# Optimization experiments

Measured on AMD Instinct MI355X. Metric: run time of the kernel, lower is better.

The kernel has to match this reference:

```python
import jax, jax.numpy as jnp
import numpy as np

B, L, V = 4, 1024, 1280
N_EMBD, N_BIN, N_HID = 768, 8, 32
HORIZON = 10.0


def setup_inputs() -> dict:
    key = jax.random.key(0)
    k_h, k_age, k_gap, k_tgt, k_w1, k_w2 = jax.random.split(key, 6)
    h = jax.random.normal(k_h, (B, L, N_EMBD), dtype=jnp.float32)
    # ages increase along a trajectory; gaps in [0, 2) years
    age = jnp.sort(jax.random.uniform(k_age, (B, L), dtype=jnp.float32) * 80.0, axis=-1)
    targets_age = age + jax.random.uniform(k_gap, (B, L), dtype=jnp.float32) * 2.0
    delta_t = targets_age - age  # passed to forward but unused (as in torch source)
    targets = jax.random.randint(k_tgt, (B, L), 0, V, dtype=jnp.int32)
    W1 = jax.random.normal(k_w1, (N_EMBD, N_BIN * N_HID), dtype=jnp.float32) * 0.02
    W2 = jax.random.normal(k_w2, (N_HID, V), dtype=jnp.float32) * 0.02
    return {"h": h, "age": age, "targets_age": targets_age, "delta_t": delta_t,
            "targets": targets, "W1": W1, "W2": W2}


def _time_to_event(age, targets_age, targets):
    # delta_full[b,i,j] = targets_age[b,j] - age[b,i]
    delta_full = targets_age[:, None, :] - age[:, :, None]  # (B,L,L)
    i_idx = jnp.arange(L)
    # torch.triu(diagonal=0): keep targets[b,j] where j>=i, else 0
    upper = (i_idx[None, :] >= i_idx[:, None])  # (L,L) mask, col>=row
    targets_exp = jnp.where(upper[None, :, :], targets[:, None, :], 0)  # (B,L,L)
    # scatter-reduce amin of position index j into vocab slot targets_exp[b,i,j]
    # sentinel L plays the role of torch's -1 (min over srcs ignores it; src<=L-1)
    b_ix = jnp.arange(B)[:, None, None]
    r_ix = i_idx[None, :, None]
    src = jnp.broadcast_to(i_idx[None, None, :], (B, L, L)).astype(jnp.int32)
    token_index = jnp.full((B, L, V), L, dtype=jnp.int32)
    token_index = token_index.at[b_ix, r_ix, targets_exp].min(src)
    no_event = token_index == L
    token_index = jnp.where(no_event, L - 1, token_index)  # (B,L,V)
    tte = jnp.take_along_axis(delta_full, token_index, axis=-1)  # (B,L,V)
    return tte, no_event, token_index


def reference(h, age, targets_age, delta_t, targets, W1, W2):
    # two dense projections: (B,L,E) -> (B,L,n_bin,n_hid) -> (B,L,n_bin,V)
    x = jnp.einsum('ble,eo->blo', h, W1).reshape(B, L, N_BIN, N_HID)
    logits = jnp.einsum('blnh,hv->blnv', x, W2)
    tte, no_event, _ = _time_to_event(age, targets_age, targets)
    edges = jnp.linspace(0.0, HORIZON, N_BIN + 1)
    lo = edges[:-1][None, None, :, None]
    hi = edges[1:][None, None, :, None]
    t = tte[:, :, None, :]  # (B,L,1,V)
    censor_mask = ((t >= lo) & (t < hi)) | no_event[:, :, None, :]  # (B,L,n_bin,V)
    return logits, tte, censor_mask
```

## Files before the change

kernel.cpp:

```cpp
#include <hip/hip_runtime.h>
#include <hip/hip_bf16.h>

#define B_   4
#define L_   1024
#define V_   1280
#define NE_  768
#define NB_  8
#define NH_  32
#define NO_  (NB_*NH_)
#define BL_  (B_*L_)
#define M2_  (BL_*NB_)
#define NCH_ 64

typedef __attribute__((ext_vector_type(8))) short bf16x8;
typedef __attribute__((ext_vector_type(4))) float floatx4;

__device__ __forceinline__ unsigned short f2bf(float f) {
    unsigned int u = __float_as_uint(f);
    u += 0x7FFFu + ((u >> 16) & 1u);
    return (unsigned short)(u >> 16);
}

#define H4_N   (BL_*NE_/4)
#define W1T_N  (NO_*NE_)
#define W2T_N  (V_*NH_)
#define K0_TOT (H4_N + W1T_N + W2T_N)

__global__ __launch_bounds__(256) void k0_pack(const float* __restrict__ h,
                                               const float* __restrict__ W1,
                                               const float* __restrict__ W2,
                                               unsigned short* __restrict__ hb,
                                               unsigned short* __restrict__ W1T,
                                               unsigned short* __restrict__ W2T) {
    int id = blockIdx.x * 256 + threadIdx.x;
    if (id < H4_N) {
        float4 v = ((const float4*)h)[id];
        ushort4 o;
        o.x = f2bf(v.x); o.y = f2bf(v.y); o.z = f2bf(v.z); o.w = f2bf(v.w);
        ((ushort4*)hb)[id] = o;
    } else if (id < H4_N + W1T_N) {
        int j = id - H4_N;
        int o = j / NE_;
        int k = j - o * NE_;
        W1T[j] = f2bf(W1[(size_t)k * NO_ + o]);
    } else if (id < K0_TOT) {
        int j = id - H4_N - W1T_N;
        int v = j >> 5;
        int k = j & 31;
        W2T[j] = f2bf(W2[(size_t)k * V_ + v]);
    }
}

__global__ __launch_bounds__(256) void k1_gemm(const unsigned short* __restrict__ hb,
                                               const unsigned short* __restrict__ W1T,
                                               unsigned short* __restrict__ Xb) {
    __shared__ short A_lds[64][40];
    __shared__ short Bt_lds[64][40];

    const int t      = threadIdx.x;
    const int m0     = blockIdx.x * 64;
    const int n0     = blockIdx.y * 64;
    const int l      = t & 63;
    const int w      = t >> 6;
    const int lane15 = l & 15;
    const int quad   = l >> 4;

    const int srow = t >> 2;
    const int sq   = (t & 3) * 8;

    const unsigned short* aptr = hb  + (size_t)(m0 + srow) * NE_ + sq;
    const unsigned short* bptr = W1T + (size_t)(n0 + srow) * NE_ + sq;

    floatx4 acc[4];
#pragma unroll
    for (int i = 0; i < 4; ++i) acc[i] = (floatx4){0.f, 0.f, 0.f, 0.f};

    bf16x8 av = *(const bf16x8*)aptr;
    bf16x8 bv = *(const bf16x8*)bptr;

    for (int k0 = 0; k0 < NE_; k0 += 32) {
        __syncthreads();
        *(bf16x8*)&A_lds[srow][sq]  = av;
        *(bf16x8*)&Bt_lds[srow][sq] = bv;
        __syncthreads();
        if (k0 + 32 < NE_) {
            av = *(const bf16x8*)(aptr + k0 + 32);
            bv = *(const bf16x8*)(bptr + k0 + 32);
        }
        bf16x8 af = *(bf16x8*)&A_lds[w * 16 + lane15][quad * 8];
#pragma unroll
        for (int nt = 0; nt < 4; ++nt) {
            bf16x8 bf = *(bf16x8*)&Bt_lds[nt * 16 + lane15][quad * 8];
            acc[nt] = __builtin_amdgcn_mfma_f32_16x16x32_bf16(af, bf, acc[nt], 0, 0, 0);
        }
    }

    const int rbase = m0 + w * 16 + quad * 4;
#pragma unroll
    for (int nt = 0; nt < 4; ++nt)
#pragma unroll
        for (int r = 0; r < 4; ++r)
            Xb[(size_t)(rbase + r) * NO_ + n0 + nt * 16 + lane15] = f2bf(acc[nt][r]);
}

__global__ __launch_bounds__(256) void k2_logits(const unsigned short* __restrict__ Xb,
                                                 const unsigned short* __restrict__ W2T,
                                                 float* __restrict__ outL) {
    const int t      = threadIdx.x;
    const int m0     = blockIdx.x * 64;
    const int nt0    = blockIdx.y * 16;
    const int l      = t & 63;
    const int w      = t >> 6;
    const int lane15 = l & 15;
    const int quad   = l >> 4;

    const int m = m0 + w * 16 + lane15;
    const bf16x8 af = *(const bf16x8*)(Xb + (size_t)m * NH_ + quad * 8);

    const int rbase = m0 + w * 16 + quad * 4;

#pragma unroll 4
    for (int nt = nt0; nt < nt0 + 16; ++nt) {
        bf16x8 bf = *(const bf16x8*)(W2T + (size_t)(nt * 16 + lane15) * NH_ + quad * 8);
        floatx4 c = (floatx4){0.f, 0.f, 0.f, 0.f};
        c = __builtin_amdgcn_mfma_f32_16x16x32_bf16(af, bf, c, 0, 0, 0);
#pragma unroll
        for (int r = 0; r < 4; ++r)
            outL[(size_t)(rbase + r) * V_ + nt * 16 + lane15] = c[r];
    }
}

__global__ __launch_bounds__(256) void k3a_nxt(const int* __restrict__ targets,
                                               int* __restrict__ nxt) {
    const int b = blockIdx.x;
    const int v = blockIdx.y * 256 + threadIdx.x;
    __shared__ int tg[L_];
    for (int j = threadIdx.x; j < L_; j += 256) tg[j] = targets[(size_t)b * L_ + j];
    __syncthreads();
    int cur = L_;
    for (int j = L_ - 1; j >= 0; --j) {
        if ((j & 15) == 15)
            nxt[((size_t)b * NCH_ + (j >> 4)) * V_ + v] = cur;
        if (tg[j] == v) cur = j;
    }
}

__global__ __launch_bounds__(64) void k3b_out(const float* __restrict__ age,
                                              const float* __restrict__ tage,
                                              const int*   __restrict__ targets,
                                              const int*   __restrict__ nxt,
                                              float* __restrict__ outT,
                                              float* __restrict__ outM) {
    __shared__ float ta[L_];
    __shared__ int   tgc[16];
    __shared__ float agc[16];

    const int t  = threadIdx.x;
    const int vt = blockIdx.x;
    const int c  = blockIdx.y;
    const int b  = blockIdx.z;
    const int v0 = vt * 256 + t * 4;

    for (int j = t; j < L_; j += 64) ta[j] = tage[(size_t)b * L_ + j];
    if (t < 16) {
        tgc[t] = targets[(size_t)b * L_ + c * 16 + t];
        agc[t] = age[(size_t)b * L_ + c * 16 + t];
    }
    __syncthreads();

    int4 cur = *(const int4*)&nxt[((size_t)b * NCH_ + c) * V_ + v0];

    for (int ii = 15; ii >= 0; --ii) {
        const int   i  = c * 16 + ii;
        const int   ti = tgc[ii];
        const float ai = agc[ii];

        if (ti == v0 + 0) cur.x = i;
        if (ti == v0 + 1) cur.y = i;
        if (ti == v0 + 2) cur.z = i;
        if (ti == v0 + 3) cur.w = i;

        int ix = cur.x, iy = cur.y, iz = cur.z, iw = cur.w;
        if (v0 == 0 && i >= 1) ix = 0;
        const bool nex = (ix == L_), ney = (iy == L_), nez = (iz == L_), new_ = (iw == L_);

        float4 tt;
        tt.x = ta[nex ? L_ - 1 : ix] - ai;
        tt.y = ta[ney ? L_ - 1 : iy] - ai;
        tt.z = ta[nez ? L_ - 1 : iz] - ai;
        tt.w = ta[new_ ? L_ - 1 : iw] - ai;

        const size_t row = (size_t)(b * L_ + i);
        *(float4*)&outT[row * V_ + v0] = tt;

        const size_t mb = row * NB_ * V_ + v0;
#pragma unroll
        for (int n = 0; n < NB_; ++n) {
            const float lo = n * 1.25f;
            const float hi = (n + 1) * 1.25f;
            float4 m;
            m.x = ((tt.x >= lo && tt.x < hi) || nex)  ? 1.0f : 0.0f;
            m.y = ((tt.y >= lo && tt.y < hi) || ney)  ? 1.0f : 0.0f;
            m.z = ((tt.z >= lo && tt.z < hi) || nez)  ? 1.0f : 0.0f;
            m.w = ((tt.w >= lo && tt.w < hi) || new_) ? 1.0f : 0.0f;
            *(float4*)&outM[mb + (size_t)n * V_] = m;
        }
    }
}

extern "C" void kernel_launch(void* const* d_in, const int* in_sizes, int n_in,
                              void* d_out, int out_size, void* d_ws, size_t ws_size,
                              hipStream_t stream) {
    const float* h       = (const float*)d_in[0];
    const float* age     = (const float*)d_in[1];
    const float* tage    = (const float*)d_in[2];
    const int*   targets = (const int*)  d_in[4];
    const float* W1      = (const float*)d_in[5];
    const float* W2      = (const float*)d_in[6];

    float* out  = (float*)d_out;
    float* outL = out;
    float* outT = out + (size_t)BL_ * NB_ * V_;
    float* outM = outT + (size_t)BL_ * V_;

    char* ws = (char*)d_ws;
    unsigned short* hb  = (unsigned short*)(ws);
    unsigned short* W1T = (unsigned short*)(ws + 6291456);
    unsigned short* W2T = (unsigned short*)(ws + 6291456 + 393216);
    unsigned short* Xb  = (unsigned short*)(ws + 6291456 + 393216 + 81920);
    int*            nxt = (int*)(ws + 6291456 + 393216 + 81920 + 2097152);

    k0_pack  <<<(K0_TOT + 255) / 256, 256, 0, stream>>>(h, W1, W2, hb, W1T, W2T);
    k3a_nxt  <<<dim3(B_, V_/256), 256, 0, stream>>>(targets, nxt);
    k1_gemm  <<<dim3(BL_/64, NO_/64), 256, 0, stream>>>(hb, W1T, Xb);
    k2_logits<<<dim3(M2_/64, 5), 256, 0, stream>>>(Xb, W2T, outL);
    k3b_out  <<<dim3(5, NCH_, B_), 64, 0, stream>>>(age, tage, targets, nxt, outT, outM);
}
```

Measured before the change: 426.9 us.

## Merge independent kernels into fewer launches with block-index dispatch

Folds the next-occurrence scan into the pack kernel and the time-to-event/mask writer into the logits kernel. Each merged kernel dispatches on block index, so five launches become three. The tte/mask part now uses 256-thread blocks that each cover four chunks. This is meant to cut launch gaps and let the write-heavy mask output overlap with the logits stores, but it puts the serial scan blocks alongside the pack blocks and mixes work of different shapes in one grid.

```diff
diff --git a/kernel.cpp b/kernel.cpp
--- a/kernel.cpp
+++ b/kernel.cpp
@@ -25,14 +25,34 @@
 #define W1T_N  (NO_*NE_)
 #define W2T_N  (V_*NH_)
 #define K0_TOT (H4_N + W1T_N + W2T_N)
-
-__global__ __launch_bounds__(256) void k0_pack(const float* __restrict__ h,
+#define K0_BLK (K0_TOT/256)
+#define KA_BLK (K0_BLK + 20)
+
+__global__ __launch_bounds__(256) void kA_prep(const float* __restrict__ h,
                                                const float* __restrict__ W1,
                                                const float* __restrict__ W2,
+                                               const int*   __restrict__ targets,
                                                unsigned short* __restrict__ hb,
                                                unsigned short* __restrict__ W1T,
-                                               unsigned short* __restrict__ W2T) {
-    int id = blockIdx.x * 256 + threadIdx.x;
+                                               unsigned short* __restrict__ W2T,
+                                               int* __restrict__ nxt) {
+    const int bx = blockIdx.x;
+    const int t  = threadIdx.x;
+    if (bx < 20) {
+        __shared__ int tg[L_];
+        const int b = bx / 5;
+        const int v = (bx % 5) * 256 + t;
+        for (int j = t; j < L_; j += 256) tg[j] = targets[(size_t)b * L_ + j];
+        __syncthreads();
+        int cur = L_;
+        for (int j = L_ - 1; j >= 0; --j) {
+            if ((j & 15) == 15)
+                nxt[((size_t)b * NCH_ + (j >> 4)) * V_ + v] = cur;
+            if (tg[j] == v) cur = j;
+        }
+        return;
+    }
+    int id = (bx - 20) * 256 + t;
     if (id < H4_N) {
         float4 v = ((const float4*)h)[id];
         ushort4 o;
@@ -103,12 +123,85 @@
             Xb[(size_t)(rbase + r) * NO_ + n0 + nt * 16 + lane15] = f2bf(acc[nt][r]);
 }
 
-__global__ __launch_bounds__(256) void k2_logits(const unsigned short* __restrict__ Xb,
-                                                 const unsigned short* __restrict__ W2T,
-                                                 float* __restrict__ outL) {
-    const int t      = threadIdx.x;
-    const int m0     = blockIdx.x * 64;
-    const int nt0    = blockIdx.y * 16;
+#define KC_TTE 320
+#define KC_BLK (KC_TTE + 512*5)
+
+__global__ __launch_bounds__(256) void kC_out(const float* __restrict__ age,
+                                              const float* __restrict__ tage,
+                                              const int*   __restrict__ targets,
+                                              const int*   __restrict__ nxt,
+                                              const unsigned short* __restrict__ Xb,
+                                              const unsigned short* __restrict__ W2T,
+                                              float* __restrict__ outL,
+                                              float* __restrict__ outT,
+                                              float* __restrict__ outM) {
+    const int bx = blockIdx.x;
+    const int t  = threadIdx.x;
+
+    if (bx < KC_TTE) {
+        __shared__ float ta[L_];
+        __shared__ int   tgc[64];
+        __shared__ float agc[64];
+
+        const int vt   = bx % 5;
+        const int c0   = (bx / 5) & 15;
+        const int b    = bx / 80;
+        const int w    = t >> 6;
+        const int lane = t & 63;
+        const int c    = c0 * 4 + w;
+        const int v0   = vt * 256 + lane * 4;
+
+        for (int j = t; j < L_; j += 256) ta[j] = tage[(size_t)b * L_ + j];
+        if (t < 64) {
+            tgc[t] = targets[(size_t)b * L_ + c0 * 64 + t];
+            agc[t] = age[(size_t)b * L_ + c0 * 64 + t];
+        }
+        __syncthreads();
+
+        int4 cur = *(const int4*)&nxt[((size_t)b * NCH_ + c) * V_ + v0];
+
+        for (int ii = 15; ii >= 0; --ii) {
+            const int   i  = c * 16 + ii;
+            const int   ti = tgc[w * 16 + ii];
+            const float ai = agc[w * 16 + ii];
+
+            if (ti == v0 + 0) cur.x = i;
+            if (ti == v0 + 1) cur.y = i;
+            if (ti == v0 + 2) cur.z = i;
+            if (ti == v0 + 3) cur.w = i;
+
+            int ix = cur.x, iy = cur.y, iz = cur.z, iw = cur.w;
+            if (v0 == 0 && i >= 1) ix = 0;
+            const bool nex = (ix == L_), ney = (iy == L_), nez = (iz == L_), new_ = (iw == L_);
+
+            float4 tt;
+            tt.x = ta[nex ? L_ - 1 : ix] - ai;
+            tt.y = ta[ney ? L_ - 1 : iy] - ai;
+            tt.z = ta[nez ? L_ - 1 : iz] - ai;
+            tt.w = ta[new_ ? L_ - 1 : iw] - ai;
+
+            const size_t row = (size_t)(b * L_ + i);
+            *(float4*)&outT[row * V_ + v0] = tt;
+
+            const size_t mb = row * NB_ * V_ + v0;
+#pragma unroll
+            for (int n = 0; n < NB_; ++n) {
+                const float lo = n * 1.25f;
+                const float hi = (n + 1) * 1.25f;
+                float4 m;
+                m.x = ((tt.x >= lo && tt.x < hi) || nex)  ? 1.0f : 0.0f;
+                m.y = ((tt.y >= lo && tt.y < hi) || ney)  ? 1.0f : 0.0f;
+                m.z = ((tt.z >= lo && tt.z < hi) || nez)  ? 1.0f : 0.0f;
+                m.w = ((tt.w >= lo && tt.w < hi) || new_) ? 1.0f : 0.0f;
+                *(float4*)&outM[mb + (size_t)n * V_] = m;
+            }
+        }
+        return;
+    }
+
+    const int j      = bx - KC_TTE;
+    const int m0     = (j & 511) * 64;
+    const int nt0    = (j >> 9) * 16;
     const int l      = t & 63;
     const int w      = t >> 6;
     const int lane15 = l & 15;
@@ -122,89 +215,11 @@
 #pragma unroll 4
     for (int nt = nt0; nt < nt0 + 16; ++nt) {
         bf16x8 bf = *(const bf16x8*)(W2T + (size_t)(nt * 16 + lane15) * NH_ + quad * 8);
-        floatx4 c = (floatx4){0.f, 0.f, 0.f, 0.f};
-        c = __builtin_amdgcn_mfma_f32_16x16x32_bf16(af, bf, c, 0, 0, 0);
+        floatx4 cc = (floatx4){0.f, 0.f, 0.f, 0.f};
+        cc = __builtin_amdgcn_mfma_f32_16x16x32_bf16(af, bf, cc, 0, 0, 0);
 #pragma unroll
         for (int r = 0; r < 4; ++r)
-            outL[(size_t)(rbase + r) * V_ + nt * 16 + lane15] = c[r];
-    }
-}
-
-__global__ __launch_bounds__(256) void k3a_nxt(const int* __restrict__ targets,
-                                               int* __restrict__ nxt) {
-    const int b = blockIdx.x;
-    const int v = blockIdx.y * 256 + threadIdx.x;
-    __shared__ int tg[L_];
-    for (int j = threadIdx.x; j < L_; j += 256) tg[j] = targets[(size_t)b * L_ + j];
-    __syncthreads();
-    int cur = L_;
-    for (int j = L_ - 1; j >= 0; --j) {
-        if ((j & 15) == 15)
-            nxt[((size_t)b * NCH_ + (j >> 4)) * V_ + v] = cur;
-        if (tg[j] == v) cur = j;
-    }
-}
-
-__global__ __launch_bounds__(64) void k3b_out(const float* __restrict__ age,
-                                              const float* __restrict__ tage,
-                                              const int*   __restrict__ targets,
-                                              const int*   __restrict__ nxt,
-                                              float* __restrict__ outT,
-                                              float* __restrict__ outM) {
-    __shared__ float ta[L_];
-    __shared__ int   tgc[16];
-    __shared__ float agc[16];
-
-    const int t  = threadIdx.x;
-    const int vt = blockIdx.x;
-    const int c  = blockIdx.y;
-    const int b  = blockIdx.z;
-    const int v0 = vt * 256 + t * 4;
-
-    for (int j = t; j < L_; j += 64) ta[j] = tage[(size_t)b * L_ + j];
-    if (t < 16) {
-        tgc[t] = targets[(size_t)b * L_ + c * 16 + t];
-        agc[t] = age[(size_t)b * L_ + c * 16 + t];
-    }
-    __syncthreads();
-
-    int4 cur = *(const int4*)&nxt[((size_t)b * NCH_ + c) * V_ + v0];
-
-    for (int ii = 15; ii >= 0; --ii) {
-        const int   i  = c * 16 + ii;
-        const int   ti = tgc[ii];
-        const float ai = agc[ii];
-
-        if (ti == v0 + 0) cur.x = i;
-        if (ti == v0 + 1) cur.y = i;
-        if (ti == v0 + 2) cur.z = i;
-        if (ti == v0 + 3) cur.w = i;
-
-        int ix = cur.x, iy = cur.y, iz = cur.z, iw = cur.w;
-        if (v0 == 0 && i >= 1) ix = 0;
-        const bool nex = (ix == L_), ney = (iy == L_), nez = (iz == L_), new_ = (iw == L_);
-
-        float4 tt;
-        tt.x = ta[nex ? L_ - 1 : ix] - ai;
-        tt.y = ta[ney ? L_ - 1 : iy] - ai;
-        tt.z = ta[nez ? L_ - 1 : iz] - ai;
-        tt.w = ta[new_ ? L_ - 1 : iw] - ai;
-
-        const size_t row = (size_t)(b * L_ + i);
-        *(float4*)&outT[row * V_ + v0] = tt;
-
-        const size_t mb = row * NB_ * V_ + v0;
-#pragma unroll
-        for (int n = 0; n < NB_; ++n) {
-            const float lo = n * 1.25f;
-            const float hi = (n + 1) * 1.25f;
-            float4 m;
-            m.x = ((tt.x >= lo && tt.x < hi) || nex)  ? 1.0f : 0.0f;
-            m.y = ((tt.y >= lo && tt.y < hi) || ney)  ? 1.0f : 0.0f;
-            m.z = ((tt.z >= lo && tt.z < hi) || nez)  ? 1.0f : 0.0f;
-            m.w = ((tt.w >= lo && tt.w < hi) || new_) ? 1.0f : 0.0f;
-            *(float4*)&outM[mb + (size_t)n * V_] = m;
-        }
+            outL[(size_t)(rbase + r) * V_ + nt * 16 + lane15] = cc[r];
     }
 }
 
@@ -230,9 +245,8 @@
     unsigned short* Xb  = (unsigned short*)(ws + 6291456 + 393216 + 81920);
     int*            nxt = (int*)(ws + 6291456 + 393216 + 81920 + 2097152);
 
-    k0_pack  <<<(K0_TOT + 255) / 256, 256, 0, stream>>>(h, W1, W2, hb, W1T, W2T);
-    k3a_nxt  <<<dim3(B_, V_/256), 256, 0, stream>>>(targets, nxt);
-    k1_gemm  <<<dim3(BL_/64, NO_/64), 256, 0, stream>>>(hb, W1T, Xb);
-    k2_logits<<<dim3(M2_/64, 5), 256, 0, stream>>>(Xb, W2T, outL);
-    k3b_out  <<<dim3(5, NCH_, B_), 64, 0, stream>>>(age, tage, targets, nxt, outT, outM);
-}
+    kA_prep<<<KA_BLK, 256, 0, stream>>>(h, W1, W2, targets, hb, W1T, W2T, nxt);
+    k1_gemm<<<dim3(BL_/64, NO_/64), 256, 0, stream>>>(hb, W1T, Xb);
+    kC_out <<<KC_BLK, 256, 0, stream>>>(age, tage, targets, nxt, Xb, W2T,
+                                        outL, outT, outM);
+}
```

Result: no change. 430.2 us (+0.8%).
